# Performance work log

Hardware: AMD Instinct MI355X
Metric: run time of the kernel (lower is better)

Reference implementation:

```python
import jax, jax.numpy as jnp
import numpy as np

B, S, D = 4, 2048, 1024
H, A = 16, 64


def setup_inputs() -> dict:
    key = jax.random.key(0)
    ks = jax.random.split(key, 9)
    return {
        "q": jax.random.normal(ks[0], (B, S, D), dtype=jnp.float32),
        "k": jax.random.normal(ks[1], (B, S, D), dtype=jnp.float32),
        "v": jax.random.normal(ks[2], (B, S, D), dtype=jnp.float32),
        "Wq": jax.random.normal(ks[3], (H, D, A), dtype=jnp.float32) * (1.0 / np.sqrt(D)),
        "bq": jax.random.normal(ks[4], (H, A), dtype=jnp.float32) * 0.01,
        "Wk": jax.random.normal(ks[5], (H, D, A), dtype=jnp.float32) * (1.0 / np.sqrt(D)),
        "bk": jax.random.normal(ks[6], (H, A), dtype=jnp.float32) * 0.01,
        "Wv": jax.random.normal(ks[7], (H, D, A), dtype=jnp.float32) * (1.0 / np.sqrt(D)),
        "bv": jax.random.normal(ks[8], (H, A), dtype=jnp.float32) * 0.01,
    }


def reference(q, k, v, Wq, bq, Wk, bk, Wv, bv):
    # Per-head linear projections (batched over heads): [B,H,S,A]
    qh = jnp.einsum("bsd,hda->bhsa", q, Wq) + bq[None, :, None, :]
    kh = jnp.einsum("bsd,hda->bhsa", k, Wk) + bk[None, :, None, :]
    vh = jnp.einsum("bsd,hda->bhsa", v, Wv) + bv[None, :, None, :]
    # NOTE: original has NO 1/sqrt(d) scaling and no mask.
    scores = jnp.einsum("bhqa,bhka->bhqk", qh, kh)  # [B,H,S,S]
    weights = jax.nn.softmax(scores, axis=-1)
    attn = jnp.einsum("bhqk,bhka->bhqa", weights, vh)  # [B,H,S,A]
    # concat heads on last dim: [B,S,H*A]
    return jnp.transpose(attn, (0, 2, 1, 3)).reshape(q.shape[0], q.shape[1], -1)
```

## Files before the change

### kernel.cpp

```cpp
#include <hip/hip_runtime.h>
#include <stdint.h>

#define B_ 4
#define S_ 2048
#define D_ 1024
#define H_ 16
#define A_ 64
#define M_ (B_*S_)
#define BH_ (B_*H_)
#define INV_LN2 1.4426950408889634f

typedef _Float16 f16x8 __attribute__((ext_vector_type(8)));
typedef float    f32x4 __attribute__((ext_vector_type(4)));

__device__ __forceinline__ uint32_t f2h(float f) {
    _Float16 h = (_Float16)f;
    return (uint32_t)__builtin_bit_cast(uint16_t, h);
}

__device__ __forceinline__ float exp2f_fast(float x) {
    return __builtin_amdgcn_exp2f(x);
}

__device__ __forceinline__ uint32_t pkrtz(float a, float b) {
    return __builtin_bit_cast(uint32_t, __builtin_amdgcn_cvt_pkrtz(a, b));
}

__device__ __forceinline__ int swz(int row, int col) {
    return (row * 64 + col) ^ ((row & 7) << 3);
}

__global__ __launch_bounds__(256) void prep_w(
    const float* __restrict__ Wq, const float* __restrict__ Wk, const float* __restrict__ Wv,
    uint16_t* __restrict__ Wt)
{
    __shared__ float tile[64][65];
    const int dt = blockIdx.x, h = blockIdx.y, p = blockIdx.z;
    const float* W = (p == 0) ? Wq : (p == 1) ? Wk : Wv;
    const float sc = (p == 0) ? INV_LN2 : 1.0f;
    const float* src = W + (h * D_ + dt * 64) * A_;
    const int t = threadIdx.x;
    const int r0 = t >> 4, c4 = (t & 15) * 4;
    #pragma unroll
    for (int i = 0; i < 4; i++) {
        int r = r0 + i * 16;
        float4 x = *(const float4*)(src + r * A_ + c4);
        tile[r][c4] = x.x; tile[r][c4 + 1] = x.y; tile[r][c4 + 2] = x.z; tile[r][c4 + 3] = x.w;
    }
    __syncthreads();
    uint16_t* dst = Wt + (p * H_ + h) * (A_ * D_) + dt * 64;
    #pragma unroll
    for (int i = 0; i < 4; i++) {
        int a = r0 + i * 16;
        int d4 = (t & 15) * 4;
        uint2 o2;
        o2.x = f2h(tile[d4][a] * sc)     | (f2h(tile[d4 + 1][a] * sc) << 16);
        o2.y = f2h(tile[d4 + 2][a] * sc) | (f2h(tile[d4 + 3][a] * sc) << 16);
        *(uint2*)(dst + a * D_ + d4) = o2;
    }
}

__global__ __launch_bounds__(512) void proj_kernel(
    const float* __restrict__ qsrc, const float* __restrict__ ksrc, const float* __restrict__ vsrc,
    const uint16_t* __restrict__ Wt,
    const float* __restrict__ bq, const float* __restrict__ bk, const float* __restrict__ bv,
    uint16_t* __restrict__ qh, uint16_t* __restrict__ kh, uint16_t* __restrict__ vpv)
{
    __shared__ __align__(16) uint16_t As[2][128 * 32];
    __shared__ __align__(16) uint16_t Bs[2][256 * 32];
    const int p = blockIdx.z, nt = blockIdx.y, mt = blockIdx.x;
    const int t = threadIdx.x, lane = t & 63, w = t >> 6;
    const int wr = w >> 2, wc = w & 3;
    const int lr = lane & 15, lg = lane >> 4;
    const int Mbase = mt * 128;
    const float* Af = (p == 0) ? qsrc : (p == 1) ? ksrc : vsrc;

    const int ar  = t >> 2;
    const int als = t & 3;
    const int afx = (ar >> 1) & 3;
    const float* asrc = Af + (size_t)(Mbase + ar) * D_ + als * 8;
    const int awoff = ar * 32 + ((als ^ afx) * 8);

    const int bslot = (t & 3) ^ (((t >> 2) >> 1) & 3);
    const uint16_t* bsrc0 = Wt + ((size_t)(p * H_ + nt * 4 + ((t >> 2) >> 6)) * A_ + ((t >> 2) & 63)) * D_ + bslot * 8;
    const uint16_t* bsrc1 = Wt + ((size_t)(p * H_ + nt * 4 + (((t >> 2) + 128) >> 6)) * A_ + ((t >> 2) & 63)) * D_ + bslot * 8;

    f32x4 acc[4][4] = {};

    #define BSTAGE(buf, kkv) do {                                                                  \
        __builtin_amdgcn_global_load_lds(bsrc0 + (kkv), (char*)(&Bs[buf][0]) + w * 1024,        16, 0, 0); \
        __builtin_amdgcn_global_load_lds(bsrc1 + (kkv), (char*)(&Bs[buf][0]) + 8192 + w * 1024, 16, 0, 0); \
    } while (0)

    #define AWRITE(buf, v0, v1) do {                                                               \
        uint4 u_;                                                                                  \
        u_.x = pkrtz((v0).x, (v0).y); u_.y = pkrtz((v0).z, (v0).w);                                \
        u_.z = pkrtz((v1).x, (v1).y); u_.w = pkrtz((v1).z, (v1).w);                                \
        *(uint4*)(&As[buf][awoff]) = u_;                                                           \
    } while (0)

    #define COMPUTE(buf) do {                                                                      \
        f16x8 af[4], bf[4];                                                                        \
        _Pragma("unroll")                                                                          \
        for (int mb = 0; mb < 4; mb++) {                                                           \
            const int r = wr * 64 + mb * 16 + lr;                                                  \
            af[mb] = *(const f16x8*)(&As[buf][r * 32 + ((lg ^ ((r >> 1) & 3)) * 8)]);              \
        }                                                                                          \
        _Pragma("unroll")                                                                          \
        for (int nb = 0; nb < 4; nb++) {                                                           \
            const int r = wc * 64 + nb * 16 + lr;                                                  \
            bf[nb] = *(const f16x8*)(&Bs[buf][r * 32 + ((lg ^ ((r >> 1) & 3)) * 8)]);              \
        }                                                                                          \
        _Pragma("unroll")                                                                          \
        for (int mb = 0; mb < 4; mb++) {                                                           \
            _Pragma("unroll")                                                                      \
            for (int nb = 0; nb < 4; nb++)                                                         \
                acc[mb][nb] = __builtin_amdgcn_mfma_f32_16x16x32_f16(af[mb], bf[nb], acc[mb][nb], 0, 0, 0); \
        }                                                                                          \
    } while (0)

    float4 e0, e1, o0, o1;
    BSTAGE(0, 0);
    __builtin_amdgcn_sched_barrier(0);
    e0 = *(const float4*)(asrc);
    e1 = *(const float4*)(asrc + 4);
    asm volatile("s_waitcnt vmcnt(0)" ::: "memory");
    AWRITE(0, e0, e1);
    __syncthreads();
    o0 = *(const float4*)(asrc + 32);
    o1 = *(const float4*)(asrc + 36);
    __builtin_amdgcn_sched_barrier(0);

    const int NKS = D_ / 32;
    for (int ks = 0; ks < NKS; ks += 2) {
        BSTAGE(1, (ks + 1) * 32);
        __builtin_amdgcn_sched_barrier(0);
        if (ks + 2 < NKS) {
            e0 = *(const float4*)(asrc + (ks + 2) * 32);
            e1 = *(const float4*)(asrc + (ks + 2) * 32 + 4);
        }
        __builtin_amdgcn_sched_barrier(0);
        COMPUTE(0);
        if (ks + 2 < NKS) asm volatile("s_waitcnt vmcnt(2)" ::: "memory");
        else              asm volatile("s_waitcnt vmcnt(0)" ::: "memory");
        __builtin_amdgcn_sched_barrier(0);
        AWRITE(1, o0, o1);
        asm volatile("s_waitcnt lgkmcnt(0)" ::: "memory");
        __builtin_amdgcn_s_barrier();
        __builtin_amdgcn_sched_barrier(0);

        if (ks + 2 < NKS) {
            BSTAGE(0, (ks + 2) * 32);
            __builtin_amdgcn_sched_barrier(0);
            if (ks + 3 < NKS) {
                o0 = *(const float4*)(asrc + (ks + 3) * 32);
                o1 = *(const float4*)(asrc + (ks + 3) * 32 + 4);
            }
            __builtin_amdgcn_sched_barrier(0);
        }
        COMPUTE(1);
        if (ks + 2 < NKS) {
            if (ks + 3 < NKS) asm volatile("s_waitcnt vmcnt(2)" ::: "memory");
            else              asm volatile("s_waitcnt vmcnt(0)" ::: "memory");
            __builtin_amdgcn_sched_barrier(0);
            AWRITE(0, e0, e1);
            asm volatile("s_waitcnt lgkmcnt(0)" ::: "memory");
            __builtin_amdgcn_s_barrier();
            __builtin_amdgcn_sched_barrier(0);
        }
    }
    #undef BSTAGE
    #undef AWRITE
    #undef COMPUTE

    const int h = nt * 4 + wc;
    const int b = Mbase >> 11;
    const int bh = b * H_ + h;
    const int sbase = Mbase & (S_ - 1);
    const float* bias = ((p == 0) ? bq : (p == 1) ? bk : bv) + h * A_;
    const float bsc = (p == 0) ? INV_LN2 : 1.0f;
    #pragma unroll
    for (int mb = 0; mb < 4; mb++) {
        #pragma unroll
        for (int nb = 0; nb < 4; nb++) {
            const int a = nb * 16 + lr;
            const float bia = bias[a] * bsc;
            const int s0 = sbase + wr * 64 + mb * 16 + 4 * lg;
            if (p < 2) {
                uint16_t* o = (p == 0) ? qh : kh;
                #pragma unroll
                for (int r = 0; r < 4; r++)
                    o[(bh * S_ + s0 + r) * A_ + a] = (uint16_t)f2h(acc[mb][nb][r] + bia);
            } else {
                const int kt2 = s0 >> 6, kv0 = s0 & 63;
                const int kb2 = kv0 >> 5, jhi = (kv0 >> 4) & 1, lg2 = (kv0 >> 2) & 3;
                uint2 pk2;
                pk2.x = f2h(acc[mb][nb][0] + bia) | (f2h(acc[mb][nb][1] + bia) << 16);
                pk2.y = f2h(acc[mb][nb][2] + bia) | (f2h(acc[mb][nb][3] + bia) << 16);
                *(uint2*)(vpv + ((size_t)((bh * 32 + kt2) * 512 + kb2 * 256 + lg2 * 64 + a)) * 8 + 4 * jhi) = pk2;
            }
        }
    }
}

__global__ __launch_bounds__(512, 8) void flash_kernel(
    const uint16_t* __restrict__ qh, const uint16_t* __restrict__ kh,
    const uint16_t* __restrict__ vpv, float* __restrict__ out)
{
    __shared__ __align__(16) uint16_t smem[24576];
    const int t = threadIdx.x, lane = t & 63, w = t >> 6;
    const int lr = lane & 15, lg = lane >> 4;

    const int flat = blockIdx.y * gridDim.x + blockIdx.x;
    const int nf = (flat & 7) * 128 + (flat >> 3);
    const int qt = nf & 15, bh = nf >> 4;
    const int b = bh >> 4, h = bh & (H_ - 1);

    f16x8 qf[2];
    {
        const uint16_t* qp = qh + (size_t)(bh * S_ + qt * 128 + w * 16 + lr) * A_ + 8 * lg;
        qf[0] = *(const f16x8*)(qp);
        qf[1] = *(const f16x8*)(qp + 32);
    }
    f16x8 ones;
    #pragma unroll
    for (int j = 0; j < 8; j++) ones[j] = (_Float16)1.0f;

    const int row0 = t >> 3;
    const int col0 = (t * 8) & 63;
    const int scol = col0 ^ ((row0 & 7) << 3);
    const uint16_t* kg = kh + (size_t)(bh * S_ + row0) * A_ + scol;
    const uint16_t* vg = vpv + (size_t)bh * (S_ * A_) + t * 8;

    f32x4 negm = {};
    f32x4 oacc[4] = {};
    f32x4 lsum = {};

    #define FSTAGE(buf, kt_) do {                                                         \
        __builtin_amdgcn_global_load_lds(kg + (size_t)(kt_) * (64 * A_),                  \
                                         smem + (buf) * 4096 + w * 512, 16, 0, 0);        \
        __builtin_amdgcn_global_load_lds(vg + (size_t)(kt_) * 4096,                       \
                                         smem + 12288 + (buf) * 4096 + w * 512, 16, 0, 0);\
    } while (0)

    const int NT = S_ / 64;
    FSTAGE(0, 0);
    FSTAGE(1, 1);

    int cur = 0;
    for (int kt = 0; kt < NT; kt++) {
        if (kt < NT - 1) asm volatile("s_waitcnt vmcnt(2)" ::: "memory");
        else             asm volatile("s_waitcnt vmcnt(0)" ::: "memory");
        __builtin_amdgcn_s_barrier();
        __builtin_amdgcn_sched_barrier(0);
        if (kt + 2 < NT) {
            int nb2 = cur + 2; if (nb2 >= 3) nb2 -= 3;
            FSTAGE(nb2, kt + 2);
        }
        __builtin_amdgcn_sched_barrier(0);
        const uint16_t* Kc = smem + cur * 4096;
        const uint16_t* Vc = smem + 12288 + cur * 4096;

        f32x4 sacc[4];
        __builtin_amdgcn_s_setprio(1);
        #pragma unroll
        for (int nb = 0; nb < 4; nb++) {
            f16x8 kf = *(const f16x8*)(Kc + swz(nb * 16 + lr, 8 * lg));
            sacc[nb] = __builtin_amdgcn_mfma_f32_16x16x32_f16(kf, qf[0], negm, 0, 0, 0);
        }
        #pragma unroll
        for (int nb = 0; nb < 4; nb++) {
            f16x8 kf = *(const f16x8*)(Kc + swz(nb * 16 + lr, 32 + 8 * lg));
            sacc[nb] = __builtin_amdgcn_mfma_f32_16x16x32_f16(kf, qf[1], sacc[nb], 0, 0, 0);
        }
        __builtin_amdgcn_s_setprio(0);

        float a0 = fmaxf(fmaxf(sacc[0][0], sacc[0][1]), sacc[0][2]);
        float a1 = fmaxf(fmaxf(sacc[0][3], sacc[1][0]), sacc[1][1]);
        float a2 = fmaxf(fmaxf(sacc[1][2], sacc[1][3]), sacc[2][0]);
        float a3 = fmaxf(fmaxf(sacc[2][1], sacc[2][2]), sacc[2][3]);
        float a4 = fmaxf(fmaxf(sacc[3][0], sacc[3][1]), sacc[3][2]);
        float pm = fmaxf(fmaxf(fmaxf(a0, a1), fmaxf(a2, a3)), fmaxf(a4, sacc[3][3]));

        if (__any(pm > 11.0f)) {
            float tm = fmaxf(pm, __shfl_xor(pm, 16));
            tm = fmaxf(tm, __shfl_xor(tm, 32));
            float delta = fmaxf(tm, 0.0f);
            float sc = exp2f_fast(-delta);
            #pragma unroll
            for (int r = 0; r < 4; r++) negm[r] -= delta;
            #pragma unroll
            for (int nb = 0; nb < 4; nb++) {
                #pragma unroll
                for (int r = 0; r < 4; r++) sacc[nb][r] -= delta;
            }
            float scr[4];
            #pragma unroll
            for (int r = 0; r < 4; r++) scr[r] = __shfl(sc, 4 * lg + r);
            #pragma unroll
            for (int r = 0; r < 4; r++) lsum[r] *= scr[r];
            #pragma unroll
            for (int nb = 0; nb < 4; nb++) {
                #pragma unroll
                for (int r = 0; r < 4; r++) oacc[nb][r] *= scr[r];
            }
        }

        f16x8 paf[2];
        #pragma unroll
        for (int kb2 = 0; kb2 < 2; kb2++) {
            float e[8];
            #pragma unroll
            for (int jh = 0; jh < 2; jh++) {
                #pragma unroll
                for (int r = 0; r < 4; r++)
                    e[jh * 4 + r] = exp2f_fast(sacc[2 * kb2 + jh][r]);
            }
            uint4 u;
            u.x = pkrtz(e[0], e[1]); u.y = pkrtz(e[2], e[3]);
            u.z = pkrtz(e[4], e[5]); u.w = pkrtz(e[6], e[7]);
            paf[kb2] = __builtin_bit_cast(f16x8, u);
        }

        __builtin_amdgcn_s_setprio(1);
        lsum = __builtin_amdgcn_mfma_f32_16x16x32_f16(paf[0], ones, lsum, 0, 0, 0);
        lsum = __builtin_amdgcn_mfma_f32_16x16x32_f16(paf[1], ones, lsum, 0, 0, 0);
        #pragma unroll
        for (int kb2 = 0; kb2 < 2; kb2++) {
            #pragma unroll
            for (int nb = 0; nb < 4; nb++) {
                f16x8 vf = *(const f16x8*)(Vc + ((kb2 * 4 + lg) * 64 + nb * 16 + lr) * 8);
                oacc[nb] = __builtin_amdgcn_mfma_f32_16x16x32_f16(paf[kb2], vf, oacc[nb], 0, 0, 0);
            }
        }
        __builtin_amdgcn_s_setprio(0);

        cur = (cur == 2) ? 0 : cur + 1;
    }
    #undef FSTAGE

    __syncthreads();
    float* outs = (float*)smem;
    #pragma unroll
    for (int r = 0; r < 4; r++) {
        const float inv = 1.0f / lsum[r];
        const int sl = w * 16 + 4 * lg + r;
        #pragma unroll
        for (int nb = 0; nb < 4; nb++)
            outs[sl * 64 + nb * 16 + lr] = oacc[nb][r] * inv;
    }
    __syncthreads();
    const int orow = t >> 4, oslot = t & 15;
    float* obase = out + (size_t)(b * S_ + qt * 128 + orow) * (H_ * A_) + h * A_ + oslot * 4;
    #pragma unroll
    for (int i = 0; i < 4; i++)
        *(float4*)(obase + (size_t)(32 * i) * (H_ * A_)) =
            *(const float4*)(outs + (orow + 32 * i) * 64 + oslot * 4);
}

extern "C" void kernel_launch(void* const* d_in, const int* in_sizes, int n_in,
                              void* d_out, int out_size, void* d_ws, size_t ws_size,
                              hipStream_t stream)
{
    const float* q  = (const float*)d_in[0];
    const float* k  = (const float*)d_in[1];
    const float* v  = (const float*)d_in[2];
    const float* Wq = (const float*)d_in[3];
    const float* bq = (const float*)d_in[4];
    const float* Wk = (const float*)d_in[5];
    const float* bk = (const float*)d_in[6];
    const float* Wv = (const float*)d_in[7];
    const float* bv = (const float*)d_in[8];
    float* out = (float*)d_out;

    uint8_t* ws = (uint8_t*)d_ws;
    const size_t SZ_H  = (size_t)BH_ * S_ * A_ * 2;
    uint16_t* qh  = (uint16_t*)(ws);
    uint16_t* kh  = (uint16_t*)(ws + SZ_H);
    uint16_t* vpv = (uint16_t*)(ws + 2 * SZ_H);
    uint16_t* Wt  = (uint16_t*)(ws + 3 * SZ_H);

    prep_w<<<dim3(16, H_, 3), 256, 0, stream>>>(Wq, Wk, Wv, Wt);
    proj_kernel<<<dim3(M_ / 128, 4, 3), 512, 0, stream>>>(q, k, v, Wt,
                                                          bq, bk, bv, qh, kh, vpv);
    flash_kernel<<<dim3(S_ / 128, BH_), 512, 0, stream>>>(qh, kh, vpv, out);
}
```

Measured before the change: 166.2 us.

## Process two 128-row query tiles per flash block to reuse K/V tiles

Each flash block now handles 256 query rows (two independent 16-row groups per wave) instead of 128, so every K/V tile staged into LDS serves twice as many queries and global K/V traffic is halved. The grid becomes 1D with half as many blocks, launch bounds drop to 4 waves-per-EU, and the output epilogue writes the two halves in sequence. This trades higher register pressure and lower occupancy, and with only 512 blocks there may be fewer blocks than needed to fill the GPU evenly.

```diff
diff --git a/kernel.cpp b/kernel.cpp
--- a/kernel.cpp
+++ b/kernel.cpp
@@ -203,7 +203,7 @@
     }
 }
 
-__global__ __launch_bounds__(512, 8) void flash_kernel(
+__global__ __launch_bounds__(512, 4) void flash_kernel(
     const uint16_t* __restrict__ qh, const uint16_t* __restrict__ kh,
     const uint16_t* __restrict__ vpv, float* __restrict__ out)
 {
@@ -211,16 +211,19 @@
     const int t = threadIdx.x, lane = t & 63, w = t >> 6;
     const int lr = lane & 15, lg = lane >> 4;
 
-    const int flat = blockIdx.y * gridDim.x + blockIdx.x;
-    const int nf = (flat & 7) * 128 + (flat >> 3);
-    const int qt = nf & 15, bh = nf >> 4;
+    const int flat = blockIdx.x;
+    const int nf = (flat & 7) * 64 + (flat >> 3);
+    const int qt = nf & 7, bh = nf >> 3;
     const int b = bh >> 4, h = bh & (H_ - 1);
 
-    f16x8 qf[2];
+    f16x8 qf0[2], qf1[2];
     {
-        const uint16_t* qp = qh + (size_t)(bh * S_ + qt * 128 + w * 16 + lr) * A_ + 8 * lg;
-        qf[0] = *(const f16x8*)(qp);
-        qf[1] = *(const f16x8*)(qp + 32);
+        const uint16_t* qp0 = qh + (size_t)(bh * S_ + qt * 256 + w * 16 + lr) * A_ + 8 * lg;
+        qf0[0] = *(const f16x8*)(qp0);
+        qf0[1] = *(const f16x8*)(qp0 + 32);
+        const uint16_t* qp1 = qp0 + (size_t)128 * A_;
+        qf1[0] = *(const f16x8*)(qp1);
+        qf1[1] = *(const f16x8*)(qp1 + 32);
     }
     f16x8 ones;
     #pragma unroll
@@ -232,9 +235,9 @@
     const uint16_t* kg = kh + (size_t)(bh * S_ + row0) * A_ + scol;
     const uint16_t* vg = vpv + (size_t)bh * (S_ * A_) + t * 8;
 
-    f32x4 negm = {};
-    f32x4 oacc[4] = {};
-    f32x4 lsum = {};
+    f32x4 negm0 = {}, negm1 = {};
+    f32x4 oacc0[4] = {}, oacc1[4] = {};
+    f32x4 lsum0 = {}, lsum1 = {};
 
     #define FSTAGE(buf, kt_) do {                                                         \
         __builtin_amdgcn_global_load_lds(kg + (size_t)(kt_) * (64 * A_),                  \
@@ -261,76 +264,136 @@
         const uint16_t* Kc = smem + cur * 4096;
         const uint16_t* Vc = smem + 12288 + cur * 4096;
 
-        f32x4 sacc[4];
+        f16x8 paf0[2], paf1[2];
+
+        {
+            f32x4 sacc[4];
+            __builtin_amdgcn_s_setprio(1);
+            #pragma unroll
+            for (int nb = 0; nb < 4; nb++) {
+                f16x8 kf = *(const f16x8*)(Kc + swz(nb * 16 + lr, 8 * lg));
+                sacc[nb] = __builtin_amdgcn_mfma_f32_16x16x32_f16(kf, qf0[0], negm0, 0, 0, 0);
+            }
+            #pragma unroll
+            for (int nb = 0; nb < 4; nb++) {
+                f16x8 kf = *(const f16x8*)(Kc + swz(nb * 16 + lr, 32 + 8 * lg));
+                sacc[nb] = __builtin_amdgcn_mfma_f32_16x16x32_f16(kf, qf0[1], sacc[nb], 0, 0, 0);
+            }
+            __builtin_amdgcn_s_setprio(0);
+            float a0 = fmaxf(fmaxf(sacc[0][0], sacc[0][1]), sacc[0][2]);
+            float a1 = fmaxf(fmaxf(sacc[0][3], sacc[1][0]), sacc[1][1]);
+            float a2 = fmaxf(fmaxf(sacc[1][2], sacc[1][3]), sacc[2][0]);
+            float a3 = fmaxf(fmaxf(sacc[2][1], sacc[2][2]), sacc[2][3]);
+            float a4 = fmaxf(fmaxf(sacc[3][0], sacc[3][1]), sacc[3][2]);
+            float pm = fmaxf(fmaxf(fmaxf(a0, a1), fmaxf(a2, a3)), fmaxf(a4, sacc[3][3]));
+            if (__any(pm > 11.0f)) {
+                float tm = fmaxf(pm, __shfl_xor(pm, 16));
+                tm = fmaxf(tm, __shfl_xor(tm, 32));
+                float delta = fmaxf(tm, 0.0f);
+                float sc = exp2f_fast(-delta);
+                #pragma unroll
+                for (int r = 0; r < 4; r++) negm0[r] -= delta;
+                #pragma unroll
+                for (int nb = 0; nb < 4; nb++) {
+                    #pragma unroll
+                    for (int r = 0; r < 4; r++) sacc[nb][r] -= delta;
+                }
+                float scr[4];
+                #pragma unroll
+                for (int r = 0; r < 4; r++) scr[r] = __shfl(sc, 4 * lg + r);
+                #pragma unroll
+                for (int r = 0; r < 4; r++) lsum0[r] *= scr[r];
+                #pragma unroll
+                for (int nb = 0; nb < 4; nb++) {
+                    #pragma unroll
+                    for (int r = 0; r < 4; r++) oacc0[nb][r] *= scr[r];
+                }
+            }
+            #pragma unroll
+            for (int kb2 = 0; kb2 < 2; kb2++) {
+                float e[8];
+                #pragma unroll
+                for (int jh = 0; jh < 2; jh++)
+                    #pragma unroll
+                    for (int r = 0; r < 4; r++)
+                        e[jh * 4 + r] = exp2f_fast(sacc[2 * kb2 + jh][r]);
+                uint4 u;
+                u.x = pkrtz(e[0], e[1]); u.y = pkrtz(e[2], e[3]);
+                u.z = pkrtz(e[4], e[5]); u.w = pkrtz(e[6], e[7]);
+                paf0[kb2] = __builtin_bit_cast(f16x8, u);
+            }
+            lsum0 = __builtin_amdgcn_mfma_f32_16x16x32_f16(paf0[0], ones, lsum0, 0, 0, 0);
+            lsum0 = __builtin_amdgcn_mfma_f32_16x16x32_f16(paf0[1], ones, lsum0, 0, 0, 0);
+        }
+
+        {
+            f32x4 sacc[4];
+            __builtin_amdgcn_s_setprio(1);
+            #pragma unroll
+            for (int nb = 0; nb < 4; nb++) {
+                f16x8 kf = *(const f16x8*)(Kc + swz(nb * 16 + lr, 8 * lg));
+                sacc[nb] = __builtin_amdgcn_mfma_f32_16x16x32_f16(kf, qf1[0], negm1, 0, 0, 0);
+            }
+            #pragma unroll
+            for (int nb = 0; nb < 4; nb++) {
+                f16x8 kf = *(const f16x8*)(Kc + swz(nb * 16 + lr, 32 + 8 * lg));
+                sacc[nb] = __builtin_amdgcn_mfma_f32_16x16x32_f16(kf, qf1[1], sacc[nb], 0, 0, 0);
+            }
+            __builtin_amdgcn_s_setprio(0);
+            float a0 = fmaxf(fmaxf(sacc[0][0], sacc[0][1]), sacc[0][2]);
+            float a1 = fmaxf(fmaxf(sacc[0][3], sacc[1][0]), sacc[1][1]);
+            float a2 = fmaxf(fmaxf(sacc[1][2], sacc[1][3]), sacc[2][0]);
+            float a3 = fmaxf(fmaxf(sacc[2][1], sacc[2][2]), sacc[2][3]);
+            float a4 = fmaxf(fmaxf(sacc[3][0], sacc[3][1]), sacc[3][2]);
+            float pm = fmaxf(fmaxf(fmaxf(a0, a1), fmaxf(a2, a3)), fmaxf(a4, sacc[3][3]));
+            if (__any(pm > 11.0f)) {
+                float tm = fmaxf(pm, __shfl_xor(pm, 16));
+                tm = fmaxf(tm, __shfl_xor(tm, 32));
+                float delta = fmaxf(tm, 0.0f);
+                float sc = exp2f_fast(-delta);
+                #pragma unroll
+                for (int r = 0; r < 4; r++) negm1[r] -= delta;
+                #pragma unroll
+                for (int nb = 0; nb < 4; nb++) {
+                    #pragma unroll
+                    for (int r = 0; r < 4; r++) sacc[nb][r] -= delta;
+                }
+                float scr[4];
+                #pragma unroll
+                for (int r = 0; r < 4; r++) scr[r] = __shfl(sc, 4 * lg + r);
+                #pragma unroll
+                for (int r = 0; r < 4; r++) lsum1[r] *= scr[r];
+                #pragma unroll
+                for (int nb = 0; nb < 4; nb++) {
+                    #pragma unroll
+                    for (int r = 0; r < 4; r++) oacc1[nb][r] *= scr[r];
+                }
+            }
+            #pragma unroll
+            for (int kb2 = 0; kb2 < 2; kb2++) {
+                float e[8];
+                #pragma unroll
+                for (int jh = 0; jh < 2; jh++)
+                    #pragma unroll
+                    for (int r = 0; r < 4; r++)
+                        e[jh * 4 + r] = exp2f_fast(sacc[2 * kb2 + jh][r]);
+                uint4 u;
+                u.x = pkrtz(e[0], e[1]); u.y = pkrtz(e[2], e[3]);
+                u.z = pkrtz(e[4], e[5]); u.w = pkrtz(e[6], e[7]);
+                paf1[kb2] = __builtin_bit_cast(f16x8, u);
+            }
+            lsum1 = __builtin_amdgcn_mfma_f32_16x16x32_f16(paf1[0], ones, lsum1, 0, 0, 0);
+            lsum1 = __builtin_amdgcn_mfma_f32_16x16x32_f16(paf1[1], ones, lsum1, 0, 0, 0);
+        }
+
         __builtin_amdgcn_s_setprio(1);
         #pragma unroll
-        for (int nb = 0; nb < 4; nb++) {
-            f16x8 kf = *(const f16x8*)(Kc + swz(nb * 16 + lr, 8 * lg));
-            sacc[nb] = __builtin_amdgcn_mfma_f32_16x16x32_f16(kf, qf[0], negm, 0, 0, 0);
-        }
-        #pragma unroll
-        for (int nb = 0; nb < 4; nb++) {
-            f16x8 kf = *(const f16x8*)(Kc + swz(nb * 16 + lr, 32 + 8 * lg));
-            sacc[nb] = __builtin_amdgcn_mfma_f32_16x16x32_f16(kf, qf[1], sacc[nb], 0, 0, 0);
-        }
-        __builtin_amdgcn_s_setprio(0);
-
-        float a0 = fmaxf(fmaxf(sacc[0][0], sacc[0][1]), sacc[0][2]);
-        float a1 = fmaxf(fmaxf(sacc[0][3], sacc[1][0]), sacc[1][1]);
-        float a2 = fmaxf(fmaxf(sacc[1][2], sacc[1][3]), sacc[2][0]);
-        float a3 = fmaxf(fmaxf(sacc[2][1], sacc[2][2]), sacc[2][3]);
-        float a4 = fmaxf(fmaxf(sacc[3][0], sacc[3][1]), sacc[3][2]);
-        float pm = fmaxf(fmaxf(fmaxf(a0, a1), fmaxf(a2, a3)), fmaxf(a4, sacc[3][3]));
-
-        if (__any(pm > 11.0f)) {
-            float tm = fmaxf(pm, __shfl_xor(pm, 16));
-            tm = fmaxf(tm, __shfl_xor(tm, 32));
-            float delta = fmaxf(tm, 0.0f);
-            float sc = exp2f_fast(-delta);
-            #pragma unroll
-            for (int r = 0; r < 4; r++) negm[r] -= delta;
-            #pragma unroll
-            for (int nb = 0; nb < 4; nb++) {
-                #pragma unroll
-                for (int r = 0; r < 4; r++) sacc[nb][r] -= delta;
-            }
-            float scr[4];
-            #pragma unroll
-            for (int r = 0; r < 4; r++) scr[r] = __shfl(sc, 4 * lg + r);
-            #pragma unroll
-            for (int r = 0; r < 4; r++) lsum[r] *= scr[r];
-            #pragma unroll
-            for (int nb = 0; nb < 4; nb++) {
-                #pragma unroll
-                for (int r = 0; r < 4; r++) oacc[nb][r] *= scr[r];
-            }
-        }
-
-        f16x8 paf[2];
-        #pragma unroll
-        for (int kb2 = 0; kb2 < 2; kb2++) {
-            float e[8];
-            #pragma unroll
-            for (int jh = 0; jh < 2; jh++) {
-                #pragma unroll
-                for (int r = 0; r < 4; r++)
-                    e[jh * 4 + r] = exp2f_fast(sacc[2 * kb2 + jh][r]);
-            }
-            uint4 u;
-            u.x = pkrtz(e[0], e[1]); u.y = pkrtz(e[2], e[3]);
-            u.z = pkrtz(e[4], e[5]); u.w = pkrtz(e[6], e[7]);
-            paf[kb2] = __builtin_bit_cast(f16x8, u);
-        }
-
-        __builtin_amdgcn_s_setprio(1);
-        lsum = __builtin_amdgcn_mfma_f32_16x16x32_f16(paf[0], ones, lsum, 0, 0, 0);
-        lsum = __builtin_amdgcn_mfma_f32_16x16x32_f16(paf[1], ones, lsum, 0, 0, 0);
-        #pragma unroll
         for (int kb2 = 0; kb2 < 2; kb2++) {
             #pragma unroll
             for (int nb = 0; nb < 4; nb++) {
                 f16x8 vf = *(const f16x8*)(Vc + ((kb2 * 4 + lg) * 64 + nb * 16 + lr) * 8);
-                oacc[nb] = __builtin_amdgcn_mfma_f32_16x16x32_f16(paf[kb2], vf, oacc[nb], 0, 0, 0);
+                oacc0[nb] = __builtin_amdgcn_mfma_f32_16x16x32_f16(paf0[kb2], vf, oacc0[nb], 0, 0, 0);
+                oacc1[nb] = __builtin_amdgcn_mfma_f32_16x16x32_f16(paf1[kb2], vf, oacc1[nb], 0, 0, 0);
             }
         }
         __builtin_amdgcn_s_setprio(0);
@@ -339,23 +402,33 @@
     }
     #undef FSTAGE
 
-    __syncthreads();
     float* outs = (float*)smem;
+    const int orow = t >> 4, oslot = t & 15;
     #pragma unroll
-    for (int r = 0; r < 4; r++) {
-        const float inv = 1.0f / lsum[r];
-        const int sl = w * 16 + 4 * lg + r;
+    for (int g = 0; g < 2; g++) {
+        __syncthreads();
         #pragma unroll
-        for (int nb = 0; nb < 4; nb++)
-            outs[sl * 64 + nb * 16 + lr] = oacc[nb][r] * inv;
-    }
-    __syncthreads();
-    const int orow = t >> 4, oslot = t & 15;
-    float* obase = out + (size_t)(b * S_ + qt * 128 + orow) * (H_ * A_) + h * A_ + oslot * 4;
-    #pragma unroll
-    for (int i = 0; i < 4; i++)
-        *(float4*)(obase + (size_t)(32 * i) * (H_ * A_)) =
-            *(const float4*)(outs + (orow + 32 * i) * 64 + oslot * 4);
+        for (int r = 0; r < 4; r++) {
+            const int sl = w * 16 + 4 * lg + r;
+            if (g == 0) {
+                const float inv = 1.0f / lsum0[r];
+                #pragma unroll
+                for (int nb = 0; nb < 4; nb++)
+                    outs[sl * 64 + nb * 16 + lr] = oacc0[nb][r] * inv;
+            } else {
+                const float inv = 1.0f / lsum1[r];
+                #pragma unroll
+                for (int nb = 0; nb < 4; nb++)
+                    outs[sl * 64 + nb * 16 + lr] = oacc1[nb][r] * inv;
+            }
+        }
+        __syncthreads();
+        float* obase = out + (size_t)(b * S_ + qt * 256 + g * 128 + orow) * (H_ * A_) + h * A_ + oslot * 4;
+        #pragma unroll
+        for (int i = 0; i < 4; i++)
+            *(float4*)(obase + (size_t)(32 * i) * (H_ * A_)) =
+                *(const float4*)(outs + (orow + 32 * i) * 64 + oslot * 4);
+    }
 }
 
 extern "C" void kernel_launch(void* const* d_in, const int* in_sizes, int n_in,
@@ -383,5 +456,5 @@
     prep_w<<<dim3(16, H_, 3), 256, 0, stream>>>(Wq, Wk, Wv, Wt);
     proj_kernel<<<dim3(M_ / 128, 4, 3), 512, 0, stream>>>(q, k, v, Wt,
                                                           bq, bk, bv, qh, kh, vpv);
-    flash_kernel<<<dim3(S_ / 128, BH_), 512, 0, stream>>>(qh, kh, vpv, out);
-}
+    flash_kernel<<<dim3(S_ / 256 * BH_), 512, 0, stream>>>(qh, kh, vpv, out);
+}
```

After: 159.7 us. 3.9% less time.

## Process two query tiles per block to reuse K/V tiles across 256 rows

Applied to the files above, without the earlier changes.

Each flash block now handles 256 query rows (two 16-row groups per wave) instead of 128, so every K/V tile staged in LDS feeds twice as many MFMAs. The global-load pipeline changes from a triple-buffered 64-key stage to double-buffered 128-key stages, with a full wait and barrier per stage. The goal is to halve K/V global and LDS traffic per query. In exchange, register use doubles, launch bounds drop to 4 waves per SIMD, LDS use grows, the grid halves to 512 blocks, and the wait before each barrier becomes blocking.

```diff
diff --git a/kernel.cpp b/kernel.cpp
--- a/kernel.cpp
+++ b/kernel.cpp
@@ -203,24 +203,27 @@
     }
 }
 
-__global__ __launch_bounds__(512, 8) void flash_kernel(
+__global__ __launch_bounds__(512, 4) void flash_kernel(
     const uint16_t* __restrict__ qh, const uint16_t* __restrict__ kh,
     const uint16_t* __restrict__ vpv, float* __restrict__ out)
 {
-    __shared__ __align__(16) uint16_t smem[24576];
+    __shared__ __align__(16) uint16_t smem[32768];
     const int t = threadIdx.x, lane = t & 63, w = t >> 6;
     const int lr = lane & 15, lg = lane >> 4;
 
-    const int flat = blockIdx.y * gridDim.x + blockIdx.x;
-    const int nf = (flat & 7) * 128 + (flat >> 3);
-    const int qt = nf & 15, bh = nf >> 4;
+    const int flat = blockIdx.x;
+    const int nf = (flat & 7) * 64 + (flat >> 3);
+    const int qt = nf & 7, bh = nf >> 3;
     const int b = bh >> 4, h = bh & (H_ - 1);
 
-    f16x8 qf[2];
+    f16x8 qf0[2], qf1[2];
     {
-        const uint16_t* qp = qh + (size_t)(bh * S_ + qt * 128 + w * 16 + lr) * A_ + 8 * lg;
-        qf[0] = *(const f16x8*)(qp);
-        qf[1] = *(const f16x8*)(qp + 32);
+        const uint16_t* qp0 = qh + (size_t)(bh * S_ + qt * 256 + w * 16 + lr) * A_ + 8 * lg;
+        qf0[0] = *(const f16x8*)(qp0);
+        qf0[1] = *(const f16x8*)(qp0 + 32);
+        const uint16_t* qp1 = qp0 + (size_t)128 * A_;
+        qf1[0] = *(const f16x8*)(qp1);
+        qf1[1] = *(const f16x8*)(qp1 + 32);
     }
     f16x8 ones;
     #pragma unroll
@@ -232,130 +235,146 @@
     const uint16_t* kg = kh + (size_t)(bh * S_ + row0) * A_ + scol;
     const uint16_t* vg = vpv + (size_t)bh * (S_ * A_) + t * 8;
 
-    f32x4 negm = {};
-    f32x4 oacc[4] = {};
-    f32x4 lsum = {};
-
-    #define FSTAGE(buf, kt_) do {                                                         \
-        __builtin_amdgcn_global_load_lds(kg + (size_t)(kt_) * (64 * A_),                  \
-                                         smem + (buf) * 4096 + w * 512, 16, 0, 0);        \
-        __builtin_amdgcn_global_load_lds(vg + (size_t)(kt_) * 4096,                       \
-                                         smem + 12288 + (buf) * 4096 + w * 512, 16, 0, 0);\
+    f32x4 negm0 = {}, negm1 = {};
+    f32x4 oacc0[4] = {}, oacc1[4] = {};
+    f32x4 lsum0 = {}, lsum1 = {};
+
+    #define FSTAGE(buf, kt_) do {                                                               \
+        __builtin_amdgcn_global_load_lds(kg + (size_t)((kt_) * 128) * A_,                       \
+                                         smem + (buf) * 8192 + w * 512, 16, 0, 0);              \
+        __builtin_amdgcn_global_load_lds(kg + (size_t)((kt_) * 128 + 64) * A_,                  \
+                                         smem + (buf) * 8192 + 4096 + w * 512, 16, 0, 0);       \
+        __builtin_amdgcn_global_load_lds(vg + (size_t)(kt_) * 8192,                             \
+                                         smem + 16384 + (buf) * 8192 + w * 512, 16, 0, 0);      \
+        __builtin_amdgcn_global_load_lds(vg + (size_t)(kt_) * 8192 + 4096,                      \
+                                         smem + 16384 + (buf) * 8192 + 4096 + w * 512, 16, 0, 0);\
     } while (0)
 
-    const int NT = S_ / 64;
+    #define GBODY(QF, NEGM, OACC, LSUM, PAF, Kc) do {                                           \
+        f32x4 sacc[4];                                                                          \
+        __builtin_amdgcn_s_setprio(1);                                                          \
+        _Pragma("unroll")                                                                       \
+        for (int nb = 0; nb < 4; nb++) {                                                        \
+            f16x8 kf = *(const f16x8*)((Kc) + swz(nb * 16 + lr, 8 * lg));                       \
+            sacc[nb] = __builtin_amdgcn_mfma_f32_16x16x32_f16(kf, (QF)[0], NEGM, 0, 0, 0);      \
+        }                                                                                       \
+        _Pragma("unroll")                                                                       \
+        for (int nb = 0; nb < 4; nb++) {                                                        \
+            f16x8 kf = *(const f16x8*)((Kc) + swz(nb * 16 + lr, 32 + 8 * lg));                  \
+            sacc[nb] = __builtin_amdgcn_mfma_f32_16x16x32_f16(kf, (QF)[1], sacc[nb], 0, 0, 0);  \
+        }                                                                                       \
+        __builtin_amdgcn_s_setprio(0);                                                          \
+        float a0 = fmaxf(fmaxf(sacc[0][0], sacc[0][1]), sacc[0][2]);                            \
+        float a1 = fmaxf(fmaxf(sacc[0][3], sacc[1][0]), sacc[1][1]);                            \
+        float a2 = fmaxf(fmaxf(sacc[1][2], sacc[1][3]), sacc[2][0]);                            \
+        float a3 = fmaxf(fmaxf(sacc[2][1], sacc[2][2]), sacc[2][3]);                            \
+        float a4 = fmaxf(fmaxf(sacc[3][0], sacc[3][1]), sacc[3][2]);                            \
+        float pm = fmaxf(fmaxf(fmaxf(a0, a1), fmaxf(a2, a3)), fmaxf(a4, sacc[3][3]));           \
+        if (__any(pm > 11.0f)) {                                                                \
+            float tm = fmaxf(pm, __shfl_xor(pm, 16));                                           \
+            tm = fmaxf(tm, __shfl_xor(tm, 32));                                                 \
+            float delta = fmaxf(tm, 0.0f);                                                      \
+            float sc = exp2f_fast(-delta);                                                      \
+            _Pragma("unroll")                                                                   \
+            for (int r = 0; r < 4; r++) (NEGM)[r] -= delta;                                     \
+            _Pragma("unroll")                                                                   \
+            for (int nb = 0; nb < 4; nb++)                                                      \
+                _Pragma("unroll")                                                               \
+                for (int r = 0; r < 4; r++) sacc[nb][r] -= delta;                               \
+            float scr[4];                                                                       \
+            _Pragma("unroll")                                                                   \
+            for (int r = 0; r < 4; r++) scr[r] = __shfl(sc, 4 * lg + r);                        \
+            _Pragma("unroll")                                                                   \
+            for (int r = 0; r < 4; r++) (LSUM)[r] *= scr[r];                                    \
+            _Pragma("unroll")                                                                   \
+            for (int nb = 0; nb < 4; nb++)                                                      \
+                _Pragma("unroll")                                                               \
+                for (int r = 0; r < 4; r++) (OACC)[nb][r] *= scr[r];                            \
+        }                                                                                       \
+        _Pragma("unroll")                                                                       \
+        for (int kb2 = 0; kb2 < 2; kb2++) {                                                     \
+            float e[8];                                                                         \
+            _Pragma("unroll")                                                                   \
+            for (int jh = 0; jh < 2; jh++)                                                      \
+                _Pragma("unroll")                                                               \
+                for (int r = 0; r < 4; r++)                                                     \
+                    e[jh * 4 + r] = exp2f_fast(sacc[2 * kb2 + jh][r]);                          \
+            uint4 u;                                                                            \
+            u.x = pkrtz(e[0], e[1]); u.y = pkrtz(e[2], e[3]);                                   \
+            u.z = pkrtz(e[4], e[5]); u.w = pkrtz(e[6], e[7]);                                   \
+            (PAF)[kb2] = __builtin_bit_cast(f16x8, u);                                          \
+        }                                                                                       \
+        (LSUM) = __builtin_amdgcn_mfma_f32_16x16x32_f16((PAF)[0], ones, LSUM, 0, 0, 0);         \
+        (LSUM) = __builtin_amdgcn_mfma_f32_16x16x32_f16((PAF)[1], ones, LSUM, 0, 0, 0);         \
+    } while (0)
+
+    const int NT = S_ / 128;
     FSTAGE(0, 0);
-    FSTAGE(1, 1);
-
-    int cur = 0;
+    asm volatile("s_waitcnt vmcnt(0)" ::: "memory");
+    __builtin_amdgcn_s_barrier();
+    __builtin_amdgcn_sched_barrier(0);
+
     for (int kt = 0; kt < NT; kt++) {
-        if (kt < NT - 1) asm volatile("s_waitcnt vmcnt(2)" ::: "memory");
-        else             asm volatile("s_waitcnt vmcnt(0)" ::: "memory");
-        __builtin_amdgcn_s_barrier();
+        const int cur = kt & 1;
+        if (kt + 1 < NT) FSTAGE(cur ^ 1, kt + 1);
         __builtin_amdgcn_sched_barrier(0);
-        if (kt + 2 < NT) {
-            int nb2 = cur + 2; if (nb2 >= 3) nb2 -= 3;
-            FSTAGE(nb2, kt + 2);
-        }
-        __builtin_amdgcn_sched_barrier(0);
-        const uint16_t* Kc = smem + cur * 4096;
-        const uint16_t* Vc = smem + 12288 + cur * 4096;
-
-        f32x4 sacc[4];
-        __builtin_amdgcn_s_setprio(1);
+
         #pragma unroll
-        for (int nb = 0; nb < 4; nb++) {
-            f16x8 kf = *(const f16x8*)(Kc + swz(nb * 16 + lr, 8 * lg));
-            sacc[nb] = __builtin_amdgcn_mfma_f32_16x16x32_f16(kf, qf[0], negm, 0, 0, 0);
-        }
+        for (int half = 0; half < 2; half++) {
+            const uint16_t* Kc = smem + cur * 8192 + half * 4096;
+            const uint16_t* Vc = smem + 16384 + cur * 8192 + half * 4096;
+            f16x8 paf0[2], paf1[2];
+            GBODY(qf0, negm0, oacc0, lsum0, paf0, Kc);
+            GBODY(qf1, negm1, oacc1, lsum1, paf1, Kc);
+            __builtin_amdgcn_s_setprio(1);
+            #pragma unroll
+            for (int kb2 = 0; kb2 < 2; kb2++) {
+                #pragma unroll
+                for (int nb = 0; nb < 4; nb++) {
+                    f16x8 vf = *(const f16x8*)(Vc + ((kb2 * 4 + lg) * 64 + nb * 16 + lr) * 8);
+                    oacc0[nb] = __builtin_amdgcn_mfma_f32_16x16x32_f16(paf0[kb2], vf, oacc0[nb], 0, 0, 0);
+                    oacc1[nb] = __builtin_amdgcn_mfma_f32_16x16x32_f16(paf1[kb2], vf, oacc1[nb], 0, 0, 0);
+                }
+            }
+            __builtin_amdgcn_s_setprio(0);
+        }
+
+        if (kt + 1 < NT) {
+            asm volatile("s_waitcnt vmcnt(0)" ::: "memory");
+            __builtin_amdgcn_s_barrier();
+            __builtin_amdgcn_sched_barrier(0);
+        }
+    }
+    #undef FSTAGE
+    #undef GBODY
+
+    float* outs = (float*)smem;
+    const int orow = t >> 4, oslot = t & 15;
+    #pragma unroll
+    for (int g = 0; g < 2; g++) {
+        __syncthreads();
         #pragma unroll
-        for (int nb = 0; nb < 4; nb++) {
-            f16x8 kf = *(const f16x8*)(Kc + swz(nb * 16 + lr, 32 + 8 * lg));
-            sacc[nb] = __builtin_amdgcn_mfma_f32_16x16x32_f16(kf, qf[1], sacc[nb], 0, 0, 0);
-        }
-        __builtin_amdgcn_s_setprio(0);
-
-        float a0 = fmaxf(fmaxf(sacc[0][0], sacc[0][1]), sacc[0][2]);
-        float a1 = fmaxf(fmaxf(sacc[0][3], sacc[1][0]), sacc[1][1]);
-        float a2 = fmaxf(fmaxf(sacc[1][2], sacc[1][3]), sacc[2][0]);
-        float a3 = fmaxf(fmaxf(sacc[2][1], sacc[2][2]), sacc[2][3]);
-        float a4 = fmaxf(fmaxf(sacc[3][0], sacc[3][1]), sacc[3][2]);
-        float pm = fmaxf(fmaxf(fmaxf(a0, a1), fmaxf(a2, a3)), fmaxf(a4, sacc[3][3]));
-
-        if (__any(pm > 11.0f)) {
-            float tm = fmaxf(pm, __shfl_xor(pm, 16));
-            tm = fmaxf(tm, __shfl_xor(tm, 32));
-            float delta = fmaxf(tm, 0.0f);
-            float sc = exp2f_fast(-delta);
-            #pragma unroll
-            for (int r = 0; r < 4; r++) negm[r] -= delta;
-            #pragma unroll
-            for (int nb = 0; nb < 4; nb++) {
+        for (int r = 0; r < 4; r++) {
+            const int sl = w * 16 + 4 * lg + r;
+            if (g == 0) {
+                const float inv = 1.0f / lsum0[r];
                 #pragma unroll
-                for (int r = 0; r < 4; r++) sacc[nb][r] -= delta;
+                for (int nb = 0; nb < 4; nb++)
+                    outs[sl * 64 + nb * 16 + lr] = oacc0[nb][r] * inv;
+            } else {
+                const float inv = 1.0f / lsum1[r];
+                #pragma unroll
+                for (int nb = 0; nb < 4; nb++)
+                    outs[sl * 64 + nb * 16 + lr] = oacc1[nb][r] * inv;
             }
-            float scr[4];
-            #pragma unroll
-            for (int r = 0; r < 4; r++) scr[r] = __shfl(sc, 4 * lg + r);
-            #pragma unroll
-            for (int r = 0; r < 4; r++) lsum[r] *= scr[r];
-            #pragma unroll
-            for (int nb = 0; nb < 4; nb++) {
-                #pragma unroll
-                for (int r = 0; r < 4; r++) oacc[nb][r] *= scr[r];
-            }
-        }
-
-        f16x8 paf[2];
+        }
+        __syncthreads();
+        float* obase = out + (size_t)(b * S_ + qt * 256 + g * 128 + orow) * (H_ * A_) + h * A_ + oslot * 4;
         #pragma unroll
-        for (int kb2 = 0; kb2 < 2; kb2++) {
-            float e[8];
-            #pragma unroll
-            for (int jh = 0; jh < 2; jh++) {
-                #pragma unroll
-                for (int r = 0; r < 4; r++)
-                    e[jh * 4 + r] = exp2f_fast(sacc[2 * kb2 + jh][r]);
-            }
-            uint4 u;
-            u.x = pkrtz(e[0], e[1]); u.y = pkrtz(e[2], e[3]);
-            u.z = pkrtz(e[4], e[5]); u.w = pkrtz(e[6], e[7]);
-            paf[kb2] = __builtin_bit_cast(f16x8, u);
-        }
-
-        __builtin_amdgcn_s_setprio(1);
-        lsum = __builtin_amdgcn_mfma_f32_16x16x32_f16(paf[0], ones, lsum, 0, 0, 0);
-        lsum = __builtin_amdgcn_mfma_f32_16x16x32_f16(paf[1], ones, lsum, 0, 0, 0);
-        #pragma unroll
-        for (int kb2 = 0; kb2 < 2; kb2++) {
-            #pragma unroll
-            for (int nb = 0; nb < 4; nb++) {
-                f16x8 vf = *(const f16x8*)(Vc + ((kb2 * 4 + lg) * 64 + nb * 16 + lr) * 8);
-                oacc[nb] = __builtin_amdgcn_mfma_f32_16x16x32_f16(paf[kb2], vf, oacc[nb], 0, 0, 0);
-            }
-        }
-        __builtin_amdgcn_s_setprio(0);
-
-        cur = (cur == 2) ? 0 : cur + 1;
-    }
-    #undef FSTAGE
-
-    __syncthreads();
-    float* outs = (float*)smem;
-    #pragma unroll
-    for (int r = 0; r < 4; r++) {
-        const float inv = 1.0f / lsum[r];
-        const int sl = w * 16 + 4 * lg + r;
-        #pragma unroll
-        for (int nb = 0; nb < 4; nb++)
-            outs[sl * 64 + nb * 16 + lr] = oacc[nb][r] * inv;
-    }
-    __syncthreads();
-    const int orow = t >> 4, oslot = t & 15;
-    float* obase = out + (size_t)(b * S_ + qt * 128 + orow) * (H_ * A_) + h * A_ + oslot * 4;
-    #pragma unroll
-    for (int i = 0; i < 4; i++)
-        *(float4*)(obase + (size_t)(32 * i) * (H_ * A_)) =
-            *(const float4*)(outs + (orow + 32 * i) * 64 + oslot * 4);
+        for (int i = 0; i < 4; i++)
+            *(float4*)(obase + (size_t)(32 * i) * (H_ * A_)) =
+                *(const float4*)(outs + (orow + 32 * i) * 64 + oslot * 4);
+    }
 }
 
 extern "C" void kernel_launch(void* const* d_in, const int* in_sizes, int n_in,
@@ -383,5 +402,5 @@
     prep_w<<<dim3(16, H_, 3), 256, 0, stream>>>(Wq, Wk, Wv, Wt);
     proj_kernel<<<dim3(M_ / 128, 4, 3), 512, 0, stream>>>(q, k, v, Wt,
                                                           bq, bk, bv, qh, kh, vpv);
-    flash_kernel<<<dim3(S_ / 128, BH_), 512, 0, stream>>>(qh, kh, vpv, out);
-}
+    flash_kernel<<<dim3(S_ / 256 * BH_), 512, 0, stream>>>(qh, kh, vpv, out);
+}
```

Measured after the change: 159.7 us (median of 2 runs). 1.04x faster.
